# Kernel optimization log

Hardware: AMD Instinct MI355X
Metric: run time of the kernel (lower is better)

## Reference

```python
import jax, jax.numpy as jnp
import numpy as np

BETA = 100.0
H = 2048
W = 2048


def setup_inputs() -> dict:
    key = jax.random.key(0)
    heatmap = jax.random.normal(key, (1, 11, H, W), dtype=jnp.float32)
    return {"heatmap": heatmap}


def _soft_argmax(hm, xx, yy):
    # hm: (..., H, W); softmax over flattened H*W, then coordinate expectation
    flat = hm.reshape(hm.shape[:-2] + (hm.shape[-2] * hm.shape[-1],))
    sm = jax.nn.softmax(flat, axis=-1).reshape(hm.shape)
    ax = jnp.sum(sm * xx, axis=(-2, -1))
    ay = jnp.sum(sm * yy, axis=(-2, -1))
    return ax, ay


def reference(heatmap):
    b, n, h, w = heatmap.shape  # structurally b=1, n=11
    dt = heatmap.dtype
    hm = heatmap * jnp.asarray(BETA, dt)
    yy = jnp.broadcast_to(jnp.arange(h, dtype=dt)[:, None], (h, w))
    xx = jnp.broadcast_to(jnp.arange(w, dtype=dt)[None, :], (h, w))

    # init: channels 9,10 (last two), full-map soft-argmax
    ax, ay = _soft_argmax(hm[0, -2:], xx, yy)  # (2,), (2,)
    out = jnp.zeros((11, 2), dt)
    out = out.at[9:11, 0].set(ax).at[9:11, 1].set(ay)
    dis0 = out[10, 1] - out[9, 1]

    channels = hm[0, :9][::-1]  # iterate i = 8 .. 0
    idxs = jnp.arange(8, -1, -1)
    rows = jnp.arange(h, dtype=dt)[:, None]  # (H,1) row coordinates for band mask

    def body(carry, xs):
        out, dis, dis_sum, dis_num = carry
        i, ch = xs
        y_ip1 = jax.lax.dynamic_slice(out, (i + 1, 1), (1, 1))[0, 0]
        y_ip2 = jax.lax.dynamic_slice(out, (i + 2, 1), (1, 1))[0, 0]
        last_y = jnp.floor(y_ip1)            # emulates .long() (y >= 0)
        tmp_dis = jnp.ceil(y_ip2 - y_ip1)
        cond = jnp.abs(tmp_dis - dis) > 0.35 * dis
        dis_sum = jnp.where(cond, dis_sum + tmp_dis, dis_sum)
        dis_num = jnp.where(cond, dis_num + 1.0, dis_num)
        dis = jnp.where(cond, dis_sum / jnp.maximum(dis_num, 1.0), dis)
        start_raw = last_y - 1.8 * dis
        end_y = jnp.round(start_raw + 0.9 * 2.0 * dis)
        start_y = jnp.round(start_raw)
        mask = ((rows >= start_y) & (rows <= end_y)).astype(dt)  # (H,1)
        ax_i, ay_i = _soft_argmax(ch * mask, xx, yy)
        row = jnp.stack([ax_i, ay_i])[None, :]  # (1,2)
        out = jax.lax.dynamic_update_slice(out, row.astype(dt), (i, jnp.zeros((), idxs.dtype)))
        return (out, dis, dis_sum, dis_num), None

    zero = jnp.zeros((), dt)
    (out, _, _, _), _ = jax.lax.scan(body, (out, dis0, zero, zero), (idxs, channels))
    return out[None]  # (1, 11, 2)
```

## Files before the change

### kernel.cpp

```cpp
#include <hip/hip_runtime.h>
#include <math.h>

#define HH 2048
#define WW 2048
#define NB 256
#define STAGE_GRID 512


__device__ __forceinline__ float wave_fmax(float v) {
#pragma unroll
  for (int m = 1; m < 64; m <<= 1) v = fmaxf(v, __shfl_xor(v, m, 64));
  return v;
}
__device__ __forceinline__ float wave_fsum(float v) {
#pragma unroll
  for (int m = 1; m < 64; m <<= 1) v += __shfl_xor(v, m, 64);
  return v;
}

__device__ float block_fmax(float v) {
  __shared__ float s[4];
  v = wave_fmax(v);
  __syncthreads();
  if ((threadIdx.x & 63) == 0) s[threadIdx.x >> 6] = v;
  __syncthreads();
  return fmaxf(fmaxf(s[0], s[1]), fmaxf(s[2], s[3]));
}

__device__ void block_fsum3(float& a, float& b, float& c) {
  __shared__ float sa[4], sb[4], sc[4];
  a = wave_fsum(a); b = wave_fsum(b); c = wave_fsum(c);
  __syncthreads();
  if ((threadIdx.x & 63) == 0) {
    int w = threadIdx.x >> 6;
    sa[w] = a; sb[w] = b; sc[w] = c;
  }
  __syncthreads();
  a = (sa[0] + sa[1]) + (sa[2] + sa[3]);
  b = (sb[0] + sb[1]) + (sb[2] + sb[3]);
  c = (sc[0] + sc[1]) + (sc[2] + sc[3]);
}

__device__ float4 wave_row_partial(const float* __restrict__ rowp) {
  const int lane = threadIdx.x & 63;
  const float4* r4 = (const float4*)rowp;
  float d[32];
  float m = -INFINITY;
#pragma unroll
  for (int p = 0; p < 8; ++p) {
    float4 v = r4[lane + 64 * p];
    d[4 * p + 0] = v.x * 100.0f;
    d[4 * p + 1] = v.y * 100.0f;
    d[4 * p + 2] = v.z * 100.0f;
    d[4 * p + 3] = v.w * 100.0f;
    m = fmaxf(m, fmaxf(fmaxf(d[4 * p], d[4 * p + 1]), fmaxf(d[4 * p + 2], d[4 * p + 3])));
  }
  float M = wave_fmax(m);
  float z = 0.0f, sx = 0.0f;
#pragma unroll
  for (int p = 0; p < 8; ++p) {
    float c0 = (float)(4 * (lane + 64 * p));
#pragma unroll
    for (int k = 0; k < 4; ++k) {
      float e = expf(d[4 * p + k] - M);
      z += e;
      sx += e * (c0 + (float)k);
    }
  }
  z = wave_fsum(z);
  sx = wave_fsum(sx);
  return make_float4(M, z, sx, 0.0f);
}

__device__ void merge_partials(const float4* __restrict__ arr, int s, int e,
                               float& M, float& Z, float& SX, float& SY) {
  float m = -INFINITY;
  for (int r = s + (int)threadIdx.x; r <= e; r += NB) m = fmaxf(m, arr[r].x);
  M = block_fmax(m);
  float z = 0.0f, sx = 0.0f, sy = 0.0f;
  for (int r = s + (int)threadIdx.x; r <= e; r += NB) {
    float4 p = arr[r];
    float w = expf(p.x - M);
    z  += w * p.y;
    sx += w * p.z;
    sy += w * p.y * (float)r;
  }
  block_fsum3(z, sx, sy);
  Z = z; SX = sx; SY = sy;
}

__device__ void finalize2(float M, float Z, float SX, float SY, int s, int e,
                          bool valid, float& ax, float& ay) {
  int nin = valid ? (e - s + 1) : 0;
  int nout = HH - nin;
  if (nout > 0) {
    float M2 = fmaxf(M, 0.0f);
    float wi = (M == M2) ? 1.0f : expf(M - M2);
    float wo = (M2 == 0.0f) ? 1.0f : expf(-M2);
    Z *= wi; SX *= wi; SY *= wi;
    float nout_e = (float)nout * (float)WW;
    float sox = (float)nout * 2096128.0f;
    float sinr = valid ? (float)(((long)(s + e) * (e - s + 1)) / 2) : 0.0f;
    float soy = (2096128.0f - sinr) * 2048.0f;
    Z  += wo * nout_e;
    SX += wo * sox;
    SY += wo * soy;
  }
  ax = SX / Z;
  ay = SY / Z;
}


__global__ __launch_bounds__(NB) void k_rows910(const float* __restrict__ heat,
                                                float* ws) {
  float4* F = (float4*)(ws + 512);
  int gw = blockIdx.x * 4 + (threadIdx.x >> 6);
  int ch = 9 + (gw >> 11);
  int r = gw & (HH - 1);
  float4 t = wave_row_partial(heat + ((size_t)ch * HH + r) * WW);
  if ((threadIdx.x & 63) == 0) F[gw] = t;
}

__global__ __launch_bounds__(NB) void k_stage(const float* __restrict__ heat,
                                              float* ws, float* __restrict__ out,
                                              int i) {
  float4* F  = (float4*)(ws + 512);
  float4* B0 = F + 4096;
  float4* B1 = B0 + HH;

  float st[28];
  if (i == 8) {
    for (int k = 0; k < 28; ++k) st[k] = 0.0f;
    float M, Z, SX, SY, ax, ay;
    merge_partials(F, 0, HH - 1, M, Z, SX, SY);
    finalize2(M, Z, SX, SY, 0, HH - 1, true, ax, ay);
    st[18] = ax; st[19] = ay;
    merge_partials(F + HH, 0, HH - 1, M, Z, SX, SY);
    finalize2(M, Z, SX, SY, 0, HH - 1, true, ax, ay);
    st[20] = ax; st[21] = ay;
    st[22] = st[21] - st[19];
    st[23] = 0.0f; st[24] = 0.0f;
  } else {
    const float* prev = ws + 32 * (i + 1);
    for (int k = 0; k < 28; ++k) st[k] = prev[k];
    const int j = i + 1;
    const float4* Bprev = (j & 1) ? B1 : B0;
    int s = (int)st[25], e = (int)st[26];
    bool valid = (st[27] != 0.0f);
    float M = -INFINITY, Z = 0.0f, SX = 0.0f, SY = 0.0f, ax, ay;
    if (valid) merge_partials(Bprev, s, e, M, Z, SX, SY);
    finalize2(M, Z, SX, SY, s, e, valid, ax, ay);
    st[2 * j] = ax; st[2 * j + 1] = ay;
  }

  if (i >= 0) {
    float y1 = st[2 * (i + 1) + 1];
    float y2 = st[2 * (i + 2) + 1];
    float dis = st[22], dsum = st[23], dnum = st[24];
    float last_y = floorf(y1);
    float tmp = ceilf(y2 - y1);
    bool cond = fabsf(tmp - dis) > 0.35f * dis;
    if (cond) { dsum += tmp; dnum += 1.0f; dis = dsum / fmaxf(dnum, 1.0f); }
    float start_raw = last_y - 1.8f * dis;
    float end_f   = rintf(start_raw + 1.8f * dis);
    float start_f = rintf(start_raw);
    int s2 = (int)fmaxf(start_f, 0.0f);
    int e2 = (int)fminf(end_f, (float)(HH - 1));
    bool bvalid = (s2 <= e2) && (end_f >= 0.0f) && (start_f <= (float)(HH - 1));
    st[22] = dis; st[23] = dsum; st[24] = dnum;
    st[25] = (float)s2; st[26] = (float)e2; st[27] = bvalid ? 1.0f : 0.0f;

    float4* Bcur = (i & 1) ? B1 : B0;
    if (bvalid) {
      const int wid = (int)(blockIdx.x * 4) + (threadIdx.x >> 6);
      for (int r = s2 + wid; r <= e2; r += (int)gridDim.x * 4) {
        float4 t = wave_row_partial(heat + ((size_t)i * HH + r) * WW);
        if ((threadIdx.x & 63) == 0) Bcur[r] = t;
      }
    }
    if (blockIdx.x == 0 && threadIdx.x == 0) {
      float* slot = ws + 32 * i;
      for (int k = 0; k < 28; ++k) slot[k] = st[k];
    }
  } else {
    if (blockIdx.x == 0 && threadIdx.x < 22) out[threadIdx.x] = st[threadIdx.x];
  }
}

extern "C" void kernel_launch(void* const* d_in, const int* in_sizes, int n_in,
                              void* d_out, int out_size, void* d_ws, size_t ws_size,
                              hipStream_t stream) {
  const float* heat = (const float*)d_in[0];
  float* out = (float*)d_out;
  float* ws = (float*)d_ws;
  hipLaunchKernelGGL(k_rows910, dim3(1024), dim3(NB), 0, stream, heat, ws);
  for (int i = 8; i >= 0; --i) {
    hipLaunchKernelGGL(k_stage, dim3(STAGE_GRID), dim3(NB), 0, stream, heat, ws, out, i);
  }
  hipLaunchKernelGGL(k_stage, dim3(1), dim3(NB), 0, stream, heat, ws, out, -1);
}
```

Measured before the change: 243.1 us.

## Precompute row partials for all channels and run dependent chain in one block

Instead of launching one kernel per sequential stage that computes row softmax partials only for the selected band, all row partials for all 11 channels are computed upfront in one fully parallel launch. A single 1024-thread block then walks the 9-step dependency chain, merging precomputed partials for each band. This removes per-stage launch and serialization overhead at the cost of reading rows outside the bands.

```diff
diff --git a/kernel.cpp b/kernel.cpp
--- a/kernel.cpp
+++ b/kernel.cpp
@@ -3,8 +3,8 @@
 
 #define HH 2048
 #define WW 2048
-#define NB 256
-#define STAGE_GRID 512
+#define NB1 256
+#define NT2 1024
 
 
 __device__ __forceinline__ float wave_fmax(float v) {
@@ -18,17 +18,20 @@
   return v;
 }
 
-__device__ float block_fmax(float v) {
-  __shared__ float s[4];
+__device__ float block_fmax16(float v) {
+  __shared__ float s[16];
   v = wave_fmax(v);
   __syncthreads();
   if ((threadIdx.x & 63) == 0) s[threadIdx.x >> 6] = v;
   __syncthreads();
-  return fmaxf(fmaxf(s[0], s[1]), fmaxf(s[2], s[3]));
+  float m = s[0];
+#pragma unroll
+  for (int k = 1; k < 16; ++k) m = fmaxf(m, s[k]);
+  return m;
 }
 
-__device__ void block_fsum3(float& a, float& b, float& c) {
-  __shared__ float sa[4], sb[4], sc[4];
+__device__ void block_fsum3_16(float& a, float& b, float& c) {
+  __shared__ float sa[16], sb[16], sc[16];
   a = wave_fsum(a); b = wave_fsum(b); c = wave_fsum(c);
   __syncthreads();
   if ((threadIdx.x & 63) == 0) {
@@ -36,9 +39,10 @@
     sa[w] = a; sb[w] = b; sc[w] = c;
   }
   __syncthreads();
-  a = (sa[0] + sa[1]) + (sa[2] + sa[3]);
-  b = (sb[0] + sb[1]) + (sb[2] + sb[3]);
-  c = (sc[0] + sc[1]) + (sc[2] + sc[3]);
+  float ra = 0.0f, rb = 0.0f, rc = 0.0f;
+#pragma unroll
+  for (int k = 0; k < 16; ++k) { ra += sa[k]; rb += sb[k]; rc += sc[k]; }
+  a = ra; b = rb; c = rc;
 }
 
 __device__ float4 wave_row_partial(const float* __restrict__ rowp) {
@@ -72,20 +76,24 @@
   return make_float4(M, z, sx, 0.0f);
 }
 
-__device__ void merge_partials(const float4* __restrict__ arr, int s, int e,
+__device__ void merge_partials(const float4* __restrict__ F, int base, int s, int e,
                                float& M, float& Z, float& SX, float& SY) {
-  float m = -INFINITY;
-  for (int r = s + (int)threadIdx.x; r <= e; r += NB) m = fmaxf(m, arr[r].x);
-  M = block_fmax(m);
+  int r0 = s + (int)threadIdx.x;
+  int r1 = r0 + NT2;
+  bool v0 = (r0 <= e), v1 = (r1 <= e);
+  float4 p0 = v0 ? F[base + r0] : make_float4(-INFINITY, 0.0f, 0.0f, 0.0f);
+  float4 p1 = v1 ? F[base + r1] : make_float4(-INFINITY, 0.0f, 0.0f, 0.0f);
+  M = block_fmax16(fmaxf(p0.x, p1.x));
   float z = 0.0f, sx = 0.0f, sy = 0.0f;
-  for (int r = s + (int)threadIdx.x; r <= e; r += NB) {
-    float4 p = arr[r];
-    float w = expf(p.x - M);
-    z  += w * p.y;
-    sx += w * p.z;
-    sy += w * p.y * (float)r;
+  if (v0) {
+    float w = expf(p0.x - M);
+    z = w * p0.y; sx = w * p0.z; sy = w * p0.y * (float)r0;
   }
-  block_fsum3(z, sx, sy);
+  if (v1) {
+    float w = expf(p1.x - M);
+    z += w * p1.y; sx += w * p1.z; sy += w * p1.y * (float)r1;
+  }
+  block_fsum3_16(z, sx, sy);
   Z = z; SX = sx; SY = sy;
 }
 
@@ -110,53 +118,31 @@
   ay = SY / Z;
 }
 
-
-__global__ __launch_bounds__(NB) void k_rows910(const float* __restrict__ heat,
-                                                float* ws) {
-  float4* F = (float4*)(ws + 512);
-  int gw = blockIdx.x * 4 + (threadIdx.x >> 6);
-  int ch = 9 + (gw >> 11);
-  int r = gw & (HH - 1);
-  float4 t = wave_row_partial(heat + ((size_t)ch * HH + r) * WW);
+__global__ __launch_bounds__(NB1) void k_partials(const float* __restrict__ heat,
+                                                  float4* __restrict__ F) {
+  int gw = blockIdx.x * 4 + (int)(threadIdx.x >> 6);
+  float4 t = wave_row_partial(heat + (size_t)gw * WW);
   if ((threadIdx.x & 63) == 0) F[gw] = t;
 }
 
-__global__ __launch_bounds__(NB) void k_stage(const float* __restrict__ heat,
-                                              float* ws, float* __restrict__ out,
-                                              int i) {
-  float4* F  = (float4*)(ws + 512);
-  float4* B0 = F + 4096;
-  float4* B1 = B0 + HH;
+__global__ __launch_bounds__(NT2) void k_chain(const float4* __restrict__ F,
+                                               float* __restrict__ out) {
+  float o[22];
+  float M, Z, SX, SY, ax, ay;
 
-  float st[28];
-  if (i == 8) {
-    for (int k = 0; k < 28; ++k) st[k] = 0.0f;
-    float M, Z, SX, SY, ax, ay;
-    merge_partials(F, 0, HH - 1, M, Z, SX, SY);
-    finalize2(M, Z, SX, SY, 0, HH - 1, true, ax, ay);
-    st[18] = ax; st[19] = ay;
-    merge_partials(F + HH, 0, HH - 1, M, Z, SX, SY);
-    finalize2(M, Z, SX, SY, 0, HH - 1, true, ax, ay);
-    st[20] = ax; st[21] = ay;
-    st[22] = st[21] - st[19];
-    st[23] = 0.0f; st[24] = 0.0f;
-  } else {
-    const float* prev = ws + 32 * (i + 1);
-    for (int k = 0; k < 28; ++k) st[k] = prev[k];
-    const int j = i + 1;
-    const float4* Bprev = (j & 1) ? B1 : B0;
-    int s = (int)st[25], e = (int)st[26];
-    bool valid = (st[27] != 0.0f);
-    float M = -INFINITY, Z = 0.0f, SX = 0.0f, SY = 0.0f, ax, ay;
-    if (valid) merge_partials(Bprev, s, e, M, Z, SX, SY);
-    finalize2(M, Z, SX, SY, s, e, valid, ax, ay);
-    st[2 * j] = ax; st[2 * j + 1] = ay;
-  }
+  merge_partials(F, 9 * HH, 0, HH - 1, M, Z, SX, SY);
+  finalize2(M, Z, SX, SY, 0, HH - 1, true, ax, ay);
+  o[18] = ax; o[19] = ay;
+  merge_partials(F, 10 * HH, 0, HH - 1, M, Z, SX, SY);
+  finalize2(M, Z, SX, SY, 0, HH - 1, true, ax, ay);
+  o[20] = ax; o[21] = ay;
 
-  if (i >= 0) {
-    float y1 = st[2 * (i + 1) + 1];
-    float y2 = st[2 * (i + 2) + 1];
-    float dis = st[22], dsum = st[23], dnum = st[24];
+  float dis = o[21] - o[19], dsum = 0.0f, dnum = 0.0f;
+
+#pragma unroll
+  for (int i = 8; i >= 0; --i) {
+    float y1 = o[2 * (i + 1) + 1];
+    float y2 = o[2 * (i + 2) + 1];
     float last_y = floorf(y1);
     float tmp = ceilf(y2 - y1);
     bool cond = fabsf(tmp - dis) > 0.35f * dis;
@@ -167,23 +153,16 @@
     int s2 = (int)fmaxf(start_f, 0.0f);
     int e2 = (int)fminf(end_f, (float)(HH - 1));
     bool bvalid = (s2 <= e2) && (end_f >= 0.0f) && (start_f <= (float)(HH - 1));
-    st[22] = dis; st[23] = dsum; st[24] = dnum;
-    st[25] = (float)s2; st[26] = (float)e2; st[27] = bvalid ? 1.0f : 0.0f;
 
-    float4* Bcur = (i & 1) ? B1 : B0;
-    if (bvalid) {
-      const int wid = (int)(blockIdx.x * 4) + (threadIdx.x >> 6);
-      for (int r = s2 + wid; r <= e2; r += (int)gridDim.x * 4) {
-        float4 t = wave_row_partial(heat + ((size_t)i * HH + r) * WW);
-        if ((threadIdx.x & 63) == 0) Bcur[r] = t;
-      }
-    }
-    if (blockIdx.x == 0 && threadIdx.x == 0) {
-      float* slot = ws + 32 * i;
-      for (int k = 0; k < 28; ++k) slot[k] = st[k];
-    }
-  } else {
-    if (blockIdx.x == 0 && threadIdx.x < 22) out[threadIdx.x] = st[threadIdx.x];
+    M = -INFINITY; Z = 0.0f; SX = 0.0f; SY = 0.0f;
+    if (bvalid) merge_partials(F, i * HH, s2, e2, M, Z, SX, SY);
+    finalize2(M, Z, SX, SY, s2, e2, bvalid, ax, ay);
+    o[2 * i] = ax; o[2 * i + 1] = ay;
+  }
+
+  if (threadIdx.x == 0) {
+#pragma unroll
+    for (int k = 0; k < 22; ++k) out[k] = o[k];
   }
 }
 
@@ -192,10 +171,7 @@
                               hipStream_t stream) {
   const float* heat = (const float*)d_in[0];
   float* out = (float*)d_out;
-  float* ws = (float*)d_ws;
-  hipLaunchKernelGGL(k_rows910, dim3(1024), dim3(NB), 0, stream, heat, ws);
-  for (int i = 8; i >= 0; --i) {
-    hipLaunchKernelGGL(k_stage, dim3(STAGE_GRID), dim3(NB), 0, stream, heat, ws, out, i);
-  }
-  hipLaunchKernelGGL(k_stage, dim3(1), dim3(NB), 0, stream, heat, ws, out, -1);
+  float4* F = (float4*)d_ws;
+  hipLaunchKernelGGL(k_partials, dim3(11 * HH / 4), dim3(NB1), 0, stream, heat, F);
+  hipLaunchKernelGGL(k_chain, dim3(1), dim3(NT2), 0, stream, F, out);
 }
```

Result: slower. 260.8 us (+7.3%).
